# Performance work log

Measured on AMD Instinct MI355X. Metric: run time of the kernel, lower is better.

## Reference

```python
import jax, jax.numpy as jnp
import numpy as np

DEPTH = 9                 # complete binary tree depth
N = 2 ** (DEPTH + 1) - 1  # 1023 nodes per tree (heap layout)
B = 32                    # batch of trees
E = 256                   # word_emb_dims
H = 512                   # treelstm in_dim (cell hidden size)
L = 512                   # decoder LSTM dims
V = 32000                 # vocab size
T = 64                    # max_sequence_length (greedy decode steps)


def setup_inputs() -> dict:
    key = jax.random.key(0)
    ks = jax.random.split(key, 12)
    g = lambda i, shape, s=0.02: jax.random.normal(ks[i], shape, jnp.float32) * s
    return {
        "node_feat": jax.random.randint(ks[0], (B, N), 0, V),
        "mask": jnp.ones((B, N), jnp.int32),
        # shared token embedding (node_emb_layer token_emb, also used by decoder input)
        "emb": g(1, (V, E)),
        # ChildSumTreeLSTMCell params (DGL convention)
        "W_iou": g(2, (E, 3 * H)),
        "U_iou": g(3, (H, 3 * H)),
        "b_iou": jnp.zeros((3 * H,), jnp.float32),
        "U_f_w": g(4, (H, H)),
        "U_f_b": jnp.zeros((H,), jnp.float32),
        # graph-readout -> decoder init state projections
        "hid_fc_w": g(5, (H, L)), "hid_fc_b": jnp.zeros((L,), jnp.float32),
        "cell_fc_w": g(6, (H, L)), "cell_fc_b": jnp.zeros((L,), jnp.float32),
        # decoder LSTMCell (PyTorch gate order i,f,g,o) + vocab projection
        "W_ih": g(7, (E, 4 * L)), "W_hh": g(8, (L, 4 * L)),
        "b_ih": jnp.zeros((4 * L,), jnp.float32), "b_hh": jnp.zeros((4 * L,), jnp.float32),
        "fc_w": g(9, (L, V)), "fc_b": jnp.zeros((V,), jnp.float32),
    }


def _forward(node_feat, mask, emb, W_iou, U_iou, b_iou, U_f_w, U_f_b,
             hid_fc_w, hid_fc_b, cell_fc_w, cell_fc_b,
             W_ih, W_hh, b_ih, b_hh, fc_w, fc_b):
    x = emb[node_feat]                                        # [B,N,E]
    iou_in = (x @ W_iou) * mask[..., None].astype(x.dtype)    # [B,N,3H]
    h = jnp.zeros((B, N, H), x.dtype)
    c = jnp.zeros((B, N, H), x.dtype)

    def apply_node(iou_node, c_agg):
        i, o, u = jnp.split(iou_node + b_iou, 3, axis=-1)
        i, o, u = jax.nn.sigmoid(i), jax.nn.sigmoid(o), jnp.tanh(u)
        c_new = i * u + c_agg
        return o * jnp.tanh(c_new), c_new

    # leaves first (no children -> zero aggregated cell)
    leaf = jnp.arange(2 ** DEPTH - 1, N)
    h_l, c_l = apply_node(iou_in[:, leaf], jnp.zeros((), x.dtype))
    h = h.at[:, leaf].set(h_l)
    c = c.at[:, leaf].set(c_l)

    # level-batched topological propagation (dgl.prop_nodes_topo)
    for d in range(DEPTH - 1, -1, -1):
        idx = jnp.arange(2 ** d - 1, 2 ** (d + 1) - 1)        # nodes at level d
        ch = jnp.stack([2 * idx + 1, 2 * idx + 2], axis=1)    # [n_d,2]
        h_ch, c_ch = h[:, ch], c[:, ch]                       # [B,n_d,2,H]
        h_tild = h_ch.sum(2)                                  # child-sum
        f = jax.nn.sigmoid(h_ch @ U_f_w + U_f_b)              # per-child forget gate
        c_agg = (f * c_ch).sum(2)
        h_n, c_n = apply_node(iou_in[:, idx] + h_tild @ U_iou, c_agg)
        h = h.at[:, idx].set(h_n)
        c = c.at[:, idx].set(c_n)

    mean_feats = h.mean(1)                                    # mean graph readout [B,H]
    hid = mean_feats @ hid_fc_w + hid_fc_b
    cel = mean_feats @ cell_fc_w + cell_fc_b

    def step(carry, _):
        inp, hs, cs = carry
        xt = emb[inp]                                         # [B,E]
        gates = xt @ W_ih + hs @ W_hh + b_ih + b_hh
        ig, fg, gg, og = jnp.split(gates, 4, axis=-1)
        cs = jax.nn.sigmoid(fg) * cs + jax.nn.sigmoid(ig) * jnp.tanh(gg)
        hs = jax.nn.sigmoid(og) * jnp.tanh(cs)
        logits = hs @ fc_w + fc_b                             # [B,V]
        top1 = jnp.argmax(logits, axis=-1)                    # greedy feedback
        return (top1, hs, cs), logits

    inp0 = jnp.zeros((B,), node_feat.dtype)
    _, logits_seq = jax.lax.scan(step, (inp0, hid, cel), None, length=T - 1)
    # t=0 row stays zeros, matching logits_output initialization
    return jnp.concatenate([jnp.zeros((1, B, V), x.dtype), logits_seq], axis=0)


def reference(node_feat, mask, emb, W_iou, U_iou, b_iou, U_f_w, U_f_b,
              hid_fc_w, hid_fc_b, cell_fc_w, cell_fc_b,
              W_ih, W_hh, b_ih, b_hh, fc_w, fc_b):
    return _forward(node_feat, mask, emb, W_iou, U_iou, b_iou, U_f_w, U_f_b,
                    hid_fc_w, hid_fc_b, cell_fc_w, cell_fc_b,
                    W_ih, W_hh, b_ih, b_hh, fc_w, fc_b)
```

## Files before the change

kernel.cpp:

```cpp
#include <hip/hip_runtime.h>
#include <math.h>

#define B_ 32
#define N_ 1023
#define E_ 256
#define H_ 512
#define V_ 32000
#define T_ 64
#define NBL 250

__device__ __forceinline__ float sigf(float x) { return 1.0f / (1.0f + expf(-x)); }

template<bool LEAF>
__global__ void __launch_bounds__(256)
iou_gemm_k(const int* __restrict__ node_feat, const int* __restrict__ mask,
           const float* __restrict__ emb, const float* __restrict__ Wiou,
           const float* __restrict__ Uiou, const float* __restrict__ hbuf,
           float* __restrict__ iou_out, int first, int n, int nshift)
{
    const int rows = B_ * n;
    const int K = LEAF ? E_ : (E_ + H_);
    const int rt = blockIdx.x, ct = blockIdx.y;
    const int tid = threadIdx.x;
    const int tr = tid >> 4, tc = tid & 15;

    __shared__ __align__(16) float As[8][136];
    __shared__ __align__(16) float Bs[8][136];

    float acc[8][8];
#pragma unroll
    for (int i = 0; i < 8; ++i)
#pragma unroll
        for (int j = 0; j < 8; ++j) acc[i][j] = 0.0f;

    const int lrow = tid >> 1;
    const int lkq  = (tid & 1) << 2;
    const int grow = rt * 128 + lrow;
    const bool rvalid = grow < rows;
    int tok = 0; float mval = 0.0f; int hoff1 = 0, hoff2 = 0;
    if (rvalid) {
        const int b = grow >> nshift, j = grow & (n - 1);
        const int node = first + j;
        tok  = node_feat[b * N_ + node];
        mval = (float)mask[b * N_ + node];
        if (!LEAF) {
            hoff1 = (b * N_ + 2 * node + 1) * H_;
            hoff2 = hoff1 + H_;
        }
    }
    const int bk   = tid >> 5;
    const int bcol = (tid & 31) << 2;
    const int gcol = ct * 128 + bcol;

    const int nkt = K >> 3;
    for (int kt = 0; kt < nkt; ++kt) {
        const int k0 = kt << 3;
        {
            const int kg = k0 + lkq;
            float4 v = make_float4(0.f, 0.f, 0.f, 0.f);
            if (rvalid) {
                if (LEAF || kg < E_) {
                    float4 e = *(const float4*)(emb + tok * E_ + kg);
                    v.x = e.x * mval; v.y = e.y * mval; v.z = e.z * mval; v.w = e.w * mval;
                } else {
                    const int kk = kg - E_;
                    float4 h1 = *(const float4*)(hbuf + hoff1 + kk);
                    float4 h2 = *(const float4*)(hbuf + hoff2 + kk);
                    v.x = h1.x + h2.x; v.y = h1.y + h2.y;
                    v.z = h1.z + h2.z; v.w = h1.w + h2.w;
                }
            }
            As[lkq + 0][lrow] = v.x;
            As[lkq + 1][lrow] = v.y;
            As[lkq + 2][lrow] = v.z;
            As[lkq + 3][lrow] = v.w;
        }
        {
            const int kg = k0 + bk;
            const float* src = (LEAF || kg < E_) ? (Wiou + kg * 1536 + gcol)
                                                 : (Uiou + (kg - E_) * 1536 + gcol);
            *(float4*)&Bs[bk][bcol] = *(const float4*)src;
        }
        __syncthreads();
#pragma unroll
        for (int kk = 0; kk < 8; ++kk) {
            float a[8], bb[8];
            *(float4*)&a[0]  = *(const float4*)&As[kk][tr << 3];
            *(float4*)&a[4]  = *(const float4*)&As[kk][(tr << 3) + 4];
            *(float4*)&bb[0] = *(const float4*)&Bs[kk][tc << 2];
            *(float4*)&bb[4] = *(const float4*)&Bs[kk][(tc << 2) + 64];
#pragma unroll
            for (int i = 0; i < 8; ++i)
#pragma unroll
                for (int j = 0; j < 8; ++j)
                    acc[i][j] = fmaf(a[i], bb[j], acc[i][j]);
        }
        __syncthreads();
    }
#pragma unroll
    for (int i = 0; i < 8; ++i) {
        const int r = rt * 128 + (tr << 3) + i;
        if (r < rows) {
            float* dst = iou_out + (size_t)r * 1536 + ct * 128;
            *(float4*)(dst + (tc << 2))      = make_float4(acc[i][0], acc[i][1], acc[i][2], acc[i][3]);
            *(float4*)(dst + 64 + (tc << 2)) = make_float4(acc[i][4], acc[i][5], acc[i][6], acc[i][7]);
        }
    }
}

__global__ void __launch_bounds__(256)
iou_small_k(const int* __restrict__ node_feat, const int* __restrict__ mask,
            const float* __restrict__ emb, const float* __restrict__ Wiou,
            const float* __restrict__ Uiou, const float* __restrict__ hbuf,
            float* __restrict__ iou_out, int first, int n, int nshift)
{
    const int rows = B_ * n;
    const int rt = blockIdx.x, ct = blockIdx.y;
    const int tid = threadIdx.x;
    const int tr = tid >> 4, tc = tid & 15;

    __shared__ __align__(16) float As[8][72];
    __shared__ __align__(16) float Bs[8][72];

    float acc[4][4];
#pragma unroll
    for (int i = 0; i < 4; ++i)
#pragma unroll
        for (int j = 0; j < 4; ++j) acc[i][j] = 0.0f;

    const int srow = tid & 63, skq = tid >> 6;
    const int grow = rt * 64 + srow;
    const bool rvalid = grow < rows;
    int tok = 0; float mval = 0.f; int hoff1 = 0, hoff2 = 0;
    if (rvalid) {
        const int b = grow >> nshift, j = grow & (n - 1);
        const int node = first + j;
        tok  = node_feat[b * N_ + node];
        mval = (float)mask[b * N_ + node];
        hoff1 = (b * N_ + 2 * node + 1) * H_;
        hoff2 = hoff1 + H_;
    }
    const int gcol = ct * 64 + srow;

    for (int kt = 0; kt < 96; ++kt) {
        const int k0 = kt << 3;
        {
            const int kg = k0 + (skq << 1);
            float2 v = make_float2(0.f, 0.f);
            if (rvalid) {
                if (kg < E_) {
                    float2 e = *(const float2*)(emb + tok * E_ + kg);
                    v.x = e.x * mval; v.y = e.y * mval;
                } else {
                    const int kk = kg - E_;
                    float2 h1 = *(const float2*)(hbuf + hoff1 + kk);
                    float2 h2 = *(const float2*)(hbuf + hoff2 + kk);
                    v.x = h1.x + h2.x; v.y = h1.y + h2.y;
                }
            }
            As[(skq << 1) + 0][srow] = v.x;
            As[(skq << 1) + 1][srow] = v.y;
        }
        {
            const int kg = k0 + (skq << 1);
            const float* s0 = (kg < E_) ? (Wiou + (size_t)kg * 1536 + gcol)
                                        : (Uiou + (size_t)(kg - E_) * 1536 + gcol);
            const float* s1 = ((kg + 1) < E_) ? (Wiou + (size_t)(kg + 1) * 1536 + gcol)
                                              : (Uiou + (size_t)(kg + 1 - E_) * 1536 + gcol);
            Bs[(skq << 1) + 0][srow] = *s0;
            Bs[(skq << 1) + 1][srow] = *s1;
        }
        __syncthreads();
#pragma unroll
        for (int kk = 0; kk < 8; ++kk) {
            float a[4], bb[4];
            *(float4*)&a[0]  = *(const float4*)&As[kk][tr << 2];
            *(float4*)&bb[0] = *(const float4*)&Bs[kk][tc << 2];
#pragma unroll
            for (int i = 0; i < 4; ++i)
#pragma unroll
                for (int j = 0; j < 4; ++j)
                    acc[i][j] = fmaf(a[i], bb[j], acc[i][j]);
        }
        __syncthreads();
    }
#pragma unroll
    for (int i = 0; i < 4; ++i) {
        const int r = rt * 64 + (tr << 2) + i;
        if (r < rows)
            *(float4*)(iou_out + (size_t)r * 1536 + ct * 64 + (tc << 2)) =
                make_float4(acc[i][0], acc[i][1], acc[i][2], acc[i][3]);
    }
}

__global__ void __launch_bounds__(256)
fagg_gemm_k(const float* __restrict__ hbuf, const float* __restrict__ cbuf,
            const float* __restrict__ Ufw, const float* __restrict__ Ufb,
            float* __restrict__ cagg, int first, int n, int nshift)
{
    const int rows = 64 * n;
    const int rt = blockIdx.x, ct = blockIdx.y;
    const int tid = threadIdx.x;
    const int tr = tid >> 4, tc = tid & 15;

    __shared__ __align__(16) float As[8][136];
    __shared__ __align__(16) float Bs[8][136];

    float acc[8][8];
#pragma unroll
    for (int i = 0; i < 8; ++i)
#pragma unroll
        for (int j = 0; j < 8; ++j) acc[i][j] = 0.0f;

    const int lrow = tid >> 1;
    const int lkq  = (tid & 1) << 2;
    const int grow = rt * 128 + lrow;
    const bool rvalid = grow < rows;
    int hoff = 0;
    if (rvalid) {
        const int bj = grow >> 1, s = grow & 1;
        const int b = bj >> nshift, j = bj & (n - 1);
        const int node = first + j;
        hoff = (b * N_ + 2 * node + 1 + s) * H_;
    }
    const int bk   = tid >> 5;
    const int bcol = (tid & 31) << 2;
    const int gcol = ct * 128 + bcol;

    for (int kt = 0; kt < 64; ++kt) {
        const int k0 = kt << 3;
        {
            const int kg = k0 + lkq;
            float4 v = make_float4(0.f, 0.f, 0.f, 0.f);
            if (rvalid) v = *(const float4*)(hbuf + hoff + kg);
            As[lkq + 0][lrow] = v.x;
            As[lkq + 1][lrow] = v.y;
            As[lkq + 2][lrow] = v.z;
            As[lkq + 3][lrow] = v.w;
        }
        {
            const int kg = k0 + bk;
            *(float4*)&Bs[bk][bcol] = *(const float4*)(Ufw + kg * H_ + gcol);
        }
        __syncthreads();
#pragma unroll
        for (int kk = 0; kk < 8; ++kk) {
            float a[8], bb[8];
            *(float4*)&a[0]  = *(const float4*)&As[kk][tr << 3];
            *(float4*)&a[4]  = *(const float4*)&As[kk][(tr << 3) + 4];
            *(float4*)&bb[0] = *(const float4*)&Bs[kk][tc << 2];
            *(float4*)&bb[4] = *(const float4*)&Bs[kk][(tc << 2) + 64];
#pragma unroll
            for (int i = 0; i < 8; ++i)
#pragma unroll
                for (int j = 0; j < 8; ++j)
                    acc[i][j] = fmaf(a[i], bb[j], acc[i][j]);
        }
        __syncthreads();
    }
#pragma unroll
    for (int p = 0; p < 4; ++p) {
        const int r0 = rt * 128 + (tr << 3) + 2 * p;
        if (r0 < rows) {
            const int bj = r0 >> 1;
            const int b = bj >> nshift, j = bj & (n - 1);
            const int node = first + j;
            const float* c1 = cbuf + (b * N_ + 2 * node + 1) * H_ + ct * 128;
            const float* c2 = c1 + H_;
            float* dst = cagg + bj * H_ + ct * 128;
#pragma unroll
            for (int g = 0; g < 2; ++g) {
                const int off = (g ? 64 : 0) + (tc << 2);
                const int jb = g * 4;
                float4 cc1 = *(const float4*)(c1 + off);
                float4 cc2 = *(const float4*)(c2 + off);
                float4 bbv = *(const float4*)(Ufb + ct * 128 + off);
                float4 res;
                res.x = sigf(acc[2*p][jb+0] + bbv.x) * cc1.x + sigf(acc[2*p+1][jb+0] + bbv.x) * cc2.x;
                res.y = sigf(acc[2*p][jb+1] + bbv.y) * cc1.y + sigf(acc[2*p+1][jb+1] + bbv.y) * cc2.y;
                res.z = sigf(acc[2*p][jb+2] + bbv.z) * cc1.z + sigf(acc[2*p+1][jb+2] + bbv.z) * cc2.z;
                res.w = sigf(acc[2*p][jb+3] + bbv.w) * cc1.w + sigf(acc[2*p+1][jb+3] + bbv.w) * cc2.w;
                *(float4*)(dst + off) = res;
            }
        }
    }
}

__global__ void __launch_bounds__(256)
fagg_small_k(const float* __restrict__ hbuf, const float* __restrict__ cbuf,
             const float* __restrict__ Ufw, const float* __restrict__ Ufb,
             float* __restrict__ cagg, int first, int n, int nshift)
{
    const int rows = 64 * n;
    const int rt = blockIdx.x, ct = blockIdx.y;
    const int tid = threadIdx.x;
    const int tr = tid >> 4, tc = tid & 15;

    __shared__ __align__(16) float As[8][72];
    __shared__ __align__(16) float Bs[8][72];

    float acc[4][4];
#pragma unroll
    for (int i = 0; i < 4; ++i)
#pragma unroll
        for (int j = 0; j < 4; ++j) acc[i][j] = 0.0f;

    const int srow = tid & 63, skq = tid >> 6;
    const int grow = rt * 64 + srow;
    const bool rvalid = grow < rows;
    int hoff = 0;
    if (rvalid) {
        const int bj = grow >> 1, s = grow & 1;
        const int b = bj >> nshift, j = bj & (n - 1);
        const int node = first + j;
        hoff = (b * N_ + 2 * node + 1 + s) * H_;
    }
    const int gcol = ct * 64 + srow;

    for (int kt = 0; kt < 64; ++kt) {
        const int k0 = kt << 3;
        {
            const int kg = k0 + (skq << 1);
            float2 v = make_float2(0.f, 0.f);
            if (rvalid) v = *(const float2*)(hbuf + hoff + kg);
            As[(skq << 1) + 0][srow] = v.x;
            As[(skq << 1) + 1][srow] = v.y;
        }
        {
            const int kg = k0 + (skq << 1);
            Bs[(skq << 1) + 0][srow] = Ufw[(size_t)kg * H_ + gcol];
            Bs[(skq << 1) + 1][srow] = Ufw[(size_t)(kg + 1) * H_ + gcol];
        }
        __syncthreads();
#pragma unroll
        for (int kk = 0; kk < 8; ++kk) {
            float a[4], bb[4];
            *(float4*)&a[0]  = *(const float4*)&As[kk][tr << 2];
            *(float4*)&bb[0] = *(const float4*)&Bs[kk][tc << 2];
#pragma unroll
            for (int i = 0; i < 4; ++i)
#pragma unroll
                for (int j = 0; j < 4; ++j)
                    acc[i][j] = fmaf(a[i], bb[j], acc[i][j]);
        }
        __syncthreads();
    }
#pragma unroll
    for (int p = 0; p < 2; ++p) {
        const int r0 = rt * 64 + (tr << 2) + 2 * p;
        if (r0 < rows) {
            const int bj = r0 >> 1;
            const int b = bj >> nshift, j = bj & (n - 1);
            const int node = first + j;
            const float* c1 = cbuf + (b * N_ + 2 * node + 1) * H_ + ct * 64;
            const float* c2 = c1 + H_;
            float* dst = cagg + bj * H_ + ct * 64;
            const int off = tc << 2;
            float4 cc1 = *(const float4*)(c1 + off);
            float4 cc2 = *(const float4*)(c2 + off);
            float4 bbv = *(const float4*)(Ufb + ct * 64 + off);
            float4 res;
            res.x = sigf(acc[2*p][0] + bbv.x) * cc1.x + sigf(acc[2*p+1][0] + bbv.x) * cc2.x;
            res.y = sigf(acc[2*p][1] + bbv.y) * cc1.y + sigf(acc[2*p+1][1] + bbv.y) * cc2.y;
            res.z = sigf(acc[2*p][2] + bbv.z) * cc1.z + sigf(acc[2*p+1][2] + bbv.z) * cc2.z;
            res.w = sigf(acc[2*p][3] + bbv.w) * cc1.w + sigf(acc[2*p+1][3] + bbv.w) * cc2.w;
            *(float4*)(dst + off) = res;
        }
    }
}

template<bool LEAF>
__global__ void apply_node_k(const float* __restrict__ iou,
                             const float* __restrict__ b_iou,
                             const float* __restrict__ cagg,
                             float* __restrict__ hbuf, float* __restrict__ cbuf,
                             int first, int n, int nshift)
{
    const int gid = blockIdx.x * 256 + threadIdx.x;
    if (gid >= B_ * n * 128) return;
    const int r = gid >> 7, col = (gid & 127) << 2;
    const float* row = iou + (size_t)r * 1536;
    float4 iv = *(const float4*)(row + col);
    float4 ov = *(const float4*)(row + 512 + col);
    float4 uv = *(const float4*)(row + 1024 + col);
    float4 bi = *(const float4*)(b_iou + col);
    float4 bo = *(const float4*)(b_iou + 512 + col);
    float4 bu = *(const float4*)(b_iou + 1024 + col);
    float4 ca = make_float4(0.f, 0.f, 0.f, 0.f);
    if (!LEAF) ca = *(const float4*)(cagg + r * H_ + col);
    float4 cn, hn;
    cn.x = sigf(iv.x + bi.x) * tanhf(uv.x + bu.x) + ca.x;
    cn.y = sigf(iv.y + bi.y) * tanhf(uv.y + bu.y) + ca.y;
    cn.z = sigf(iv.z + bi.z) * tanhf(uv.z + bu.z) + ca.z;
    cn.w = sigf(iv.w + bi.w) * tanhf(uv.w + bu.w) + ca.w;
    hn.x = sigf(ov.x + bo.x) * tanhf(cn.x);
    hn.y = sigf(ov.y + bo.y) * tanhf(cn.y);
    hn.z = sigf(ov.z + bo.z) * tanhf(cn.z);
    hn.w = sigf(ov.w + bo.w) * tanhf(cn.w);
    const int b = r >> nshift, j = r & (n - 1);
    const int node = first + j;
    const size_t o = (size_t)(b * N_ + node) * H_ + col;
    *(float4*)(cbuf + o) = cn;
    *(float4*)(hbuf + o) = hn;
}

__global__ void mean_part_k(const float* __restrict__ hbuf, float* __restrict__ mpart)
{
    const int bid = blockIdx.x;
    const int b = bid >> 3, chunk = bid & 7;
    const int tid = threadIdx.x;
    const int n0 = chunk * 128;
    const int n1 = (n0 + 128 < N_) ? (n0 + 128) : N_;
    float s0 = 0.f, s1 = 0.f;
    for (int nn = n0; nn < n1; ++nn) {
        const float* p = hbuf + (size_t)(b * N_ + nn) * H_;
        s0 += p[tid];
        s1 += p[tid + 256];
    }
    mpart[(bid << 9) + tid]       = s0;
    mpart[(bid << 9) + tid + 256] = s1;
}

__global__ void mean_fin_k(const float* __restrict__ mpart, float* __restrict__ mf)
{
    const int gid = blockIdx.x * 256 + threadIdx.x;
    const int b = gid >> 9, k = gid & 511;
    float s = 0.f;
#pragma unroll
    for (int c = 0; c < 8; ++c) s += mpart[(((b << 3) + c) << 9) + k];
    mf[gid] = s * (1.0f / 1023.0f);
}

__global__ void hidcel_k(const float* __restrict__ mf,
                         const float* __restrict__ hw, const float* __restrict__ hb,
                         const float* __restrict__ cw, const float* __restrict__ cb,
                         float* __restrict__ hs0, float* __restrict__ cs)
{
    const int gid = blockIdx.x * 256 + threadIdx.x;
    const int which = gid >> 14;
    const int b = (gid >> 9) & 31, l = gid & 511;
    const float* W = which ? cw : hw;
    float acc = which ? cb[l] : hb[l];
#pragma unroll 8
    for (int k = 0; k < H_; ++k) acc = fmaf(mf[b * H_ + k], W[k * H_ + l], acc);
    if (which) cs[b * H_ + l] = acc; else hs0[b * H_ + l] = acc;
}

__global__ void __launch_bounds__(256)
wtrans_k(const float* __restrict__ W_ih, const float* __restrict__ W_hh,
         float* __restrict__ Wt)
{
    __shared__ float t[64][33];
    const int k0 = blockIdx.x * 32;
    const int g0 = blockIdx.y * 64;
    const int tid = threadIdx.x;
    for (int idx = tid; idx < 2048; idx += 256) {
        const int kk = idx >> 6, gg = idx & 63;
        const int k = k0 + kk;
        t[gg][kk] = (k < E_) ? W_ih[(size_t)k * 2048 + g0 + gg]
                             : W_hh[(size_t)(k - E_) * 2048 + g0 + gg];
    }
    __syncthreads();
    for (int idx = tid; idx < 2048; idx += 256) {
        const int gg = idx >> 5, kk = idx & 31;
        Wt[(size_t)(g0 + gg) * 768 + k0 + kk] = t[gg][kk];
    }
}

__global__ void __launch_bounds__(256)
lstm_step_k(const float* __restrict__ emb, const float* __restrict__ Wt,
            const float* __restrict__ b_ih, const float* __restrict__ b_hh,
            const float* __restrict__ pval, const int* __restrict__ pidx,
            const float* __restrict__ hs_in, float* __restrict__ hs_out,
            float* __restrict__ cs, int t)
{
    __shared__ __align__(16) float xh[8][776];
    __shared__ __align__(16) float part[4][8][8][4];
    __shared__ float rv[256];
    __shared__ int   ri[256];
    __shared__ int   tokS[8];
    const int tid = threadIdx.x;
    const int bg  = blockIdx.y;

    if (t == 1) {
        if (tid < 8) tokS[tid] = 0;
    } else {
        const int bs = tid >> 5, th = tid & 31;
        const int b = bg * 8 + bs;
        float bv = -INFINITY; int bi = 0x7fffffff;
        for (int p = th; p < NBL; p += 32) {
            const float v = pval[b * NBL + p];
            const int  ix = pidx[b * NBL + p];
            if (v > bv || (v == bv && ix < bi)) { bv = v; bi = ix; }
        }
        rv[tid] = bv; ri[tid] = bi;
        __syncthreads();
        if (tid < 8) {
            float Bv = -INFINITY; int Bi = 0x7fffffff;
#pragma unroll
            for (int c = 0; c < 32; ++c) {
                const float v = rv[tid * 32 + c];
                const int  ix = ri[tid * 32 + c];
                if (v > Bv || (v == Bv && ix < Bi)) { Bv = v; Bi = ix; }
            }
            tokS[tid] = Bi;
        }
    }
    __syncthreads();

    for (int idx = tid; idx < 8 * E_; idx += 256) {
        const int b = idx >> 8, k = idx & 255;
        xh[b][k] = emb[(size_t)tokS[b] * E_ + k];
    }
    for (int idx = tid; idx < 8 * H_; idx += 256) {
        const int b = idx >> 9, k = idx & 511;
        xh[b][E_ + k] = hs_in[(size_t)(bg * 8 + b) * H_ + k];
    }
    __syncthreads();

    const int ks = tid >> 6;
    const int lane = tid & 63;
    const int bi = lane >> 3, li = lane & 7;
    const int l = blockIdx.x * 8 + li;
    float ai = 0.f, af = 0.f, ag = 0.f, ao = 0.f;
    const int k0 = ks * 192;
    const float* wi = Wt + (size_t)(l)        * 768 + k0;
    const float* wf = Wt + (size_t)(512 + l)  * 768 + k0;
    const float* wg = Wt + (size_t)(1024 + l) * 768 + k0;
    const float* wo = Wt + (size_t)(1536 + l) * 768 + k0;
    const float* xp = &xh[bi][k0];
#pragma unroll 4
    for (int kk = 0; kk < 192; kk += 4) {
        const float4 xv = *(const float4*)(xp + kk);
        const float4 w0 = *(const float4*)(wi + kk);
        const float4 w1 = *(const float4*)(wf + kk);
        const float4 w2 = *(const float4*)(wg + kk);
        const float4 w3 = *(const float4*)(wo + kk);
        ai = fmaf(xv.x, w0.x, ai); ai = fmaf(xv.y, w0.y, ai);
        ai = fmaf(xv.z, w0.z, ai); ai = fmaf(xv.w, w0.w, ai);
        af = fmaf(xv.x, w1.x, af); af = fmaf(xv.y, w1.y, af);
        af = fmaf(xv.z, w1.z, af); af = fmaf(xv.w, w1.w, af);
        ag = fmaf(xv.x, w2.x, ag); ag = fmaf(xv.y, w2.y, ag);
        ag = fmaf(xv.z, w2.z, ag); ag = fmaf(xv.w, w2.w, ag);
        ao = fmaf(xv.x, w3.x, ao); ao = fmaf(xv.y, w3.y, ao);
        ao = fmaf(xv.z, w3.z, ao); ao = fmaf(xv.w, w3.w, ao);
    }
    part[ks][bi][li][0] = ai;
    part[ks][bi][li][1] = af;
    part[ks][bi][li][2] = ag;
    part[ks][bi][li][3] = ao;
    __syncthreads();

    if (tid < 64) {
        const int b2 = tid >> 3, l2i = tid & 7;
        const int l2 = blockIdx.x * 8 + l2i;
        const int b = bg * 8 + b2;
        float s0 = 0.f, s1 = 0.f, s2 = 0.f, s3 = 0.f;
#pragma unroll
        for (int q = 0; q < 4; ++q) {
            s0 += part[q][b2][l2i][0];
            s1 += part[q][b2][l2i][1];
            s2 += part[q][b2][l2i][2];
            s3 += part[q][b2][l2i][3];
        }
        const float gi = s0 + b_ih[l2]        + b_hh[l2];
        const float gf = s1 + b_ih[512 + l2]  + b_hh[512 + l2];
        const float gg = s2 + b_ih[1024 + l2] + b_hh[1024 + l2];
        const float go = s3 + b_ih[1536 + l2] + b_hh[1536 + l2];
        const float co = cs[b * H_ + l2];
        const float cn = sigf(gf) * co + sigf(gi) * tanhf(gg);
        cs[b * H_ + l2] = cn;
        hs_out[b * H_ + l2] = sigf(go) * tanhf(cn);
    }
}

__global__ void __launch_bounds__(256)
logits_part_k(const float* __restrict__ fc_w, const float* __restrict__ hs,
              float* __restrict__ partial)
{
    __shared__ __align__(16) float sm[256 * 36];
    const int tid = threadIdx.x;
    const int blk = blockIdx.x;
    const int kh  = blockIdx.y;

    for (int idx = tid; idx < B_ * 256; idx += 256) {
        const int b = idx & 31, k = idx >> 5;
        sm[k * 36 + b] = hs[b * H_ + kh * 256 + k];
    }
    __syncthreads();

    const int w8   = (tid >> 6) << 3;
    const int lane = tid & 63;
    const int col  = (blk << 7) + (lane << 1);

    float acc[8][2];
#pragma unroll
    for (int i = 0; i < 8; ++i) { acc[i][0] = 0.f; acc[i][1] = 0.f; }

    const float* wp = fc_w + (size_t)(kh * 256) * V_ + col;
    const float* hp = sm + w8;
    float2 wreg[8];
#pragma unroll
    for (int j = 0; j < 8; ++j) wreg[j] = *(const float2*)(wp + (size_t)j * V_);
    for (int kb = 0; kb < 32; ++kb) {
        float2 wnxt[8];
        if (kb < 31) {
            const float* wq = wp + (size_t)((kb + 1) << 3) * V_;
#pragma unroll
            for (int j = 0; j < 8; ++j) wnxt[j] = *(const float2*)(wq + (size_t)j * V_);
        }
#pragma unroll
        for (int j = 0; j < 8; ++j) {
            const float* hq = hp + ((kb << 3) + j) * 36;
            float hv[8];
            *(float4*)&hv[0] = *(const float4*)(hq);
            *(float4*)&hv[4] = *(const float4*)(hq + 4);
#pragma unroll
            for (int i = 0; i < 8; ++i) {
                acc[i][0] = fmaf(hv[i], wreg[j].x, acc[i][0]);
                acc[i][1] = fmaf(hv[i], wreg[j].y, acc[i][1]);
            }
        }
        if (kb < 31) {
#pragma unroll
            for (int j = 0; j < 8; ++j) wreg[j] = wnxt[j];
        }
    }
#pragma unroll
    for (int i = 0; i < 8; ++i) {
        float* dst = partial + (size_t)(kh * B_ + w8 + i) * V_ + col;
        *(float2*)dst = make_float2(acc[i][0], acc[i][1]);
    }
}

__global__ void __launch_bounds__(256)
logits_fin_k(const float* __restrict__ partial, const float* __restrict__ fc_b,
             float* __restrict__ out_t, float* __restrict__ pval,
             int* __restrict__ pidx)
{
    __shared__ float rv[256];
    __shared__ int   ri[256];
    const int tid = threadIdx.x, blk = blockIdx.x;
    const int b = tid >> 3, cg = (tid & 7) << 4;
    const int colbase = (blk << 7) + cg;

    const float* p0 = partial + (size_t)b * V_ + colbase;
    const float* p1 = partial + (size_t)(B_ + b) * V_ + colbase;
    const float* bp = fc_b + colbase;
    float* op = out_t + (size_t)b * V_ + colbase;

    float bv = -INFINITY; int bi = 0;
#pragma unroll
    for (int q = 0; q < 4; ++q) {
        float4 a = *(const float4*)(p0 + (q << 2));
        float4 c = *(const float4*)(p1 + (q << 2));
        float4 d = *(const float4*)(bp + (q << 2));
        float4 v;
        v.x = a.x + c.x + d.x; v.y = a.y + c.y + d.y;
        v.z = a.z + c.z + d.z; v.w = a.w + c.w + d.w;
        *(float4*)(op + (q << 2)) = v;
        const int c0 = cg + (q << 2);
        if (v.x > bv) { bv = v.x; bi = c0 + 0; }
        if (v.y > bv) { bv = v.y; bi = c0 + 1; }
        if (v.z > bv) { bv = v.z; bi = c0 + 2; }
        if (v.w > bv) { bv = v.w; bi = c0 + 3; }
    }
    rv[tid] = bv; ri[tid] = bi;
    __syncthreads();
    if (tid < B_) {
        float Bv = -INFINITY; int Bi = 0;
#pragma unroll
        for (int q = 0; q < 8; ++q) {
            const float v = rv[(tid << 3) + q];
            if (v > Bv) { Bv = v; Bi = ri[(tid << 3) + q]; }
        }
        pval[tid * NBL + blk] = Bv;
        pidx[tid * NBL + blk] = (blk << 7) + Bi;
    }
}

extern "C" void kernel_launch(void* const* d_in, const int* in_sizes, int n_in,
                              void* d_out, int out_size, void* d_ws, size_t ws_size,
                              hipStream_t stream)
{
    (void)in_sizes; (void)n_in; (void)out_size; (void)ws_size;
    const int*   node_feat = (const int*)  d_in[0];
    const int*   mask      = (const int*)  d_in[1];
    const float* emb       = (const float*)d_in[2];
    const float* W_iou     = (const float*)d_in[3];
    const float* U_iou     = (const float*)d_in[4];
    const float* b_iou     = (const float*)d_in[5];
    const float* U_f_w     = (const float*)d_in[6];
    const float* U_f_b     = (const float*)d_in[7];
    const float* hid_fc_w  = (const float*)d_in[8];
    const float* hid_fc_b  = (const float*)d_in[9];
    const float* cell_fc_w = (const float*)d_in[10];
    const float* cell_fc_b = (const float*)d_in[11];
    const float* W_ih      = (const float*)d_in[12];
    const float* W_hh      = (const float*)d_in[13];
    const float* b_ih      = (const float*)d_in[14];
    const float* b_hh      = (const float*)d_in[15];
    const float* fc_w      = (const float*)d_in[16];
    const float* fc_b      = (const float*)d_in[17];
    float* out = (float*)d_out;

    float* ws      = (float*)d_ws;
    float* iou_buf = ws;
    float* cagg    = ws + 12582912;
    float* hbuf    = ws + 16777216;
    float* cbuf    = ws + 33538048;
    float* mf      = ws + 50298880;
    float* hsb     = ws + 50315264;
    float* csb     = ws + 50348032;
    float* pval    = ws + 50364416;
    int*   pidx    = (int*)(ws + 50372416);
    float* mpart   = iou_buf;
    float* partial = iou_buf + 262144;
    float* Wt      = iou_buf + 2359296;

    for (int chunk = 0; chunk < 2; ++chunk) {
        const int first = 511 + 256 * chunk;
        dim3 g(64, 12);
        iou_gemm_k<true><<<g, 256, 0, stream>>>(node_feat, mask, emb, W_iou, U_iou,
                                                hbuf, iou_buf, first, 256, 8);
        apply_node_k<true><<<4096, 256, 0, stream>>>(iou_buf, b_iou, cagg,
                                                     hbuf, cbuf, first, 256, 8);
    }
    for (int d = 8; d >= 0; --d) {
        const int n = 1 << d, first = n - 1;
        if (n <= 64) {
            dim3 gf((64 * n + 63) / 64, 8);
            fagg_small_k<<<gf, 256, 0, stream>>>(hbuf, cbuf, U_f_w, U_f_b, cagg, first, n, d);
            dim3 gi((32 * n + 63) / 64, 24);
            iou_small_k<<<gi, 256, 0, stream>>>(node_feat, mask, emb, W_iou, U_iou,
                                                hbuf, iou_buf, first, n, d);
        } else {
            dim3 gf((64 * n + 127) / 128, 4);
            fagg_gemm_k<<<gf, 256, 0, stream>>>(hbuf, cbuf, U_f_w, U_f_b, cagg, first, n, d);
            dim3 gi((32 * n + 127) / 128, 12);
            iou_gemm_k<false><<<gi, 256, 0, stream>>>(node_feat, mask, emb, W_iou, U_iou,
                                                      hbuf, iou_buf, first, n, d);
        }
        apply_node_k<false><<<16 * n, 256, 0, stream>>>(iou_buf, b_iou, cagg,
                                                        hbuf, cbuf, first, n, d);
    }
    mean_part_k<<<256, 256, 0, stream>>>(hbuf, mpart);
    mean_fin_k<<<64, 256, 0, stream>>>(mpart, mf);
    hidcel_k<<<128, 256, 0, stream>>>(mf, hid_fc_w, hid_fc_b, cell_fc_w, cell_fc_b, hsb, csb);
    dim3 gw(24, 32);
    wtrans_k<<<gw, 256, 0, stream>>>(W_ih, W_hh, Wt);
    hipMemsetAsync(d_out, 0, (size_t)B_ * V_ * sizeof(float), stream);
    for (int t = 1; t < T_; ++t) {
        const float* hs_in  = hsb + ((t - 1) & 1) * (B_ * H_);
        float*       hs_out = hsb + (t & 1) * (B_ * H_);
        dim3 gl(64, 4);
        lstm_step_k<<<gl, 256, 0, stream>>>(emb, Wt, b_ih, b_hh,
                                            pval, pidx, hs_in, hs_out, csb, t);
        dim3 gp(NBL, 2);
        logits_part_k<<<gp, 256, 0, stream>>>(fc_w, hs_out, partial);
        logits_fin_k<<<NBL, 256, 0, stream>>>(partial, fc_b,
                                              out + (size_t)t * B_ * V_, pval, pidx);
    }
}
```

Before: 5.996 ms.

## Fuse iou GEMM with node apply and use nontemporal logits stores

```diff
diff --git a/kernel.cpp b/kernel.cpp
--- a/kernel.cpp
+++ b/kernel.cpp
@@ -11,12 +11,21 @@
 
 __device__ __forceinline__ float sigf(float x) { return 1.0f / (1.0f + expf(-x)); }
 
+__device__ __forceinline__ void nt_store4(float* p, float4 v)
+{
+    __builtin_nontemporal_store(v.x, p + 0);
+    __builtin_nontemporal_store(v.y, p + 1);
+    __builtin_nontemporal_store(v.z, p + 2);
+    __builtin_nontemporal_store(v.w, p + 3);
+}
+
 template<bool LEAF>
 __global__ void __launch_bounds__(256)
-iou_gemm_k(const int* __restrict__ node_feat, const int* __restrict__ mask,
-           const float* __restrict__ emb, const float* __restrict__ Wiou,
-           const float* __restrict__ Uiou, const float* __restrict__ hbuf,
-           float* __restrict__ iou_out, int first, int n, int nshift)
+iou_apply_k(const int* __restrict__ node_feat, const int* __restrict__ mask,
+            const float* __restrict__ emb, const float* __restrict__ Wiou,
+            const float* __restrict__ Uiou, const float* __restrict__ b_iou,
+            const float* __restrict__ cagg, float* __restrict__ hbuf,
+            float* __restrict__ cbuf, int first, int n, int nshift)
 {
     const int rows = B_ * n;
     const int K = LEAF ? E_ : (E_ + H_);
@@ -24,20 +33,19 @@
     const int tid = threadIdx.x;
     const int tr = tid >> 4, tc = tid & 15;
 
-    __shared__ __align__(16) float As[8][136];
-    __shared__ __align__(16) float Bs[8][136];
-
-    float acc[8][8];
-#pragma unroll
-    for (int i = 0; i < 8; ++i)
-#pragma unroll
-        for (int j = 0; j < 8; ++j) acc[i][j] = 0.0f;
-
-    const int lrow = tid >> 1;
-    const int lkq  = (tid & 1) << 2;
-    const int grow = rt * 128 + lrow;
+    __shared__ __align__(16) float As[8][72];
+    __shared__ __align__(16) float Bs[3][8][136];
+
+    float aI[4][8], aO[4][8], aU[4][8];
+#pragma unroll
+    for (int i = 0; i < 4; ++i)
+#pragma unroll
+        for (int j = 0; j < 8; ++j) { aI[i][j] = 0.f; aO[i][j] = 0.f; aU[i][j] = 0.f; }
+
+    const int srow = tid & 63, skq = tid >> 6;
+    const int grow = rt * 64 + srow;
     const bool rvalid = grow < rows;
-    int tok = 0; float mval = 0.0f; int hoff1 = 0, hoff2 = 0;
+    int tok = 0; float mval = 0.f; int hoff1 = 0, hoff2 = 0;
     if (rvalid) {
         const int b = grow >> nshift, j = grow & (n - 1);
         const int node = first + j;
@@ -56,54 +64,88 @@
     for (int kt = 0; kt < nkt; ++kt) {
         const int k0 = kt << 3;
         {
-            const int kg = k0 + lkq;
-            float4 v = make_float4(0.f, 0.f, 0.f, 0.f);
+            const int kg = k0 + (skq << 1);
+            float2 v = make_float2(0.f, 0.f);
             if (rvalid) {
                 if (LEAF || kg < E_) {
-                    float4 e = *(const float4*)(emb + tok * E_ + kg);
-                    v.x = e.x * mval; v.y = e.y * mval; v.z = e.z * mval; v.w = e.w * mval;
+                    float2 e = *(const float2*)(emb + (size_t)tok * E_ + kg);
+                    v.x = e.x * mval; v.y = e.y * mval;
                 } else {
                     const int kk = kg - E_;
-                    float4 h1 = *(const float4*)(hbuf + hoff1 + kk);
-                    float4 h2 = *(const float4*)(hbuf + hoff2 + kk);
+                    float2 h1 = *(const float2*)(hbuf + hoff1 + kk);
+                    float2 h2 = *(const float2*)(hbuf + hoff2 + kk);
                     v.x = h1.x + h2.x; v.y = h1.y + h2.y;
-                    v.z = h1.z + h2.z; v.w = h1.w + h2.w;
                 }
             }
-            As[lkq + 0][lrow] = v.x;
-            As[lkq + 1][lrow] = v.y;
-            As[lkq + 2][lrow] = v.z;
-            As[lkq + 3][lrow] = v.w;
+            As[(skq << 1) + 0][srow] = v.x;
+            As[(skq << 1) + 1][srow] = v.y;
         }
         {
             const int kg = k0 + bk;
-            const float* src = (LEAF || kg < E_) ? (Wiou + kg * 1536 + gcol)
-                                                 : (Uiou + (kg - E_) * 1536 + gcol);
-            *(float4*)&Bs[bk][bcol] = *(const float4*)src;
+            const float* src = (LEAF || kg < E_) ? (Wiou + (size_t)kg * 1536)
+                                                 : (Uiou + (size_t)(kg - E_) * 1536);
+            *(float4*)&Bs[0][bk][bcol] = *(const float4*)(src + gcol);
+            *(float4*)&Bs[1][bk][bcol] = *(const float4*)(src + 512 + gcol);
+            *(float4*)&Bs[2][bk][bcol] = *(const float4*)(src + 1024 + gcol);
         }
         __syncthreads();
 #pragma unroll
         for (int kk = 0; kk < 8; ++kk) {
-            float a[8], bb[8];
-            *(float4*)&a[0]  = *(const float4*)&As[kk][tr << 3];
-            *(float4*)&a[4]  = *(const float4*)&As[kk][(tr << 3) + 4];
-            *(float4*)&bb[0] = *(const float4*)&Bs[kk][tc << 2];
-            *(float4*)&bb[4] = *(const float4*)&Bs[kk][(tc << 2) + 64];
-#pragma unroll
-            for (int i = 0; i < 8; ++i)
-#pragma unroll
-                for (int j = 0; j < 8; ++j)
-                    acc[i][j] = fmaf(a[i], bb[j], acc[i][j]);
+            float a[4];
+            *(float4*)&a[0] = *(const float4*)&As[kk][tr << 2];
+            float bI[8], bO[8], bU[8];
+            *(float4*)&bI[0] = *(const float4*)&Bs[0][kk][tc << 3];
+            *(float4*)&bI[4] = *(const float4*)&Bs[0][kk][(tc << 3) + 4];
+            *(float4*)&bO[0] = *(const float4*)&Bs[1][kk][tc << 3];
+            *(float4*)&bO[4] = *(const float4*)&Bs[1][kk][(tc << 3) + 4];
+            *(float4*)&bU[0] = *(const float4*)&Bs[2][kk][tc << 3];
+            *(float4*)&bU[4] = *(const float4*)&Bs[2][kk][(tc << 3) + 4];
+#pragma unroll
+            for (int i = 0; i < 4; ++i)
+#pragma unroll
+                for (int j = 0; j < 8; ++j) {
+                    aI[i][j] = fmaf(a[i], bI[j], aI[i][j]);
+                    aO[i][j] = fmaf(a[i], bO[j], aO[i][j]);
+                    aU[i][j] = fmaf(a[i], bU[j], aU[i][j]);
+                }
         }
         __syncthreads();
     }
-#pragma unroll
-    for (int i = 0; i < 8; ++i) {
-        const int r = rt * 128 + (tr << 3) + i;
+
+    const int cbase = ct * 128 + (tc << 3);
+    float bI[8], bO[8], bU[8];
+    *(float4*)&bI[0] = *(const float4*)(b_iou + cbase);
+    *(float4*)&bI[4] = *(const float4*)(b_iou + cbase + 4);
+    *(float4*)&bO[0] = *(const float4*)(b_iou + 512 + cbase);
+    *(float4*)&bO[4] = *(const float4*)(b_iou + 512 + cbase + 4);
+    *(float4*)&bU[0] = *(const float4*)(b_iou + 1024 + cbase);
+    *(float4*)&bU[4] = *(const float4*)(b_iou + 1024 + cbase + 4);
+
+#pragma unroll
+    for (int p = 0; p < 4; ++p) {
+        const int r = rt * 64 + (tr << 2) + p;
         if (r < rows) {
-            float* dst = iou_out + (size_t)r * 1536 + ct * 128;
-            *(float4*)(dst + (tc << 2))      = make_float4(acc[i][0], acc[i][1], acc[i][2], acc[i][3]);
-            *(float4*)(dst + 64 + (tc << 2)) = make_float4(acc[i][4], acc[i][5], acc[i][6], acc[i][7]);
+            const int b = r >> nshift, j = r & (n - 1);
+            const int node = first + j;
+            float ca[8];
+            if (LEAF) {
+#pragma unroll
+                for (int e = 0; e < 8; ++e) ca[e] = 0.f;
+            } else {
+                *(float4*)&ca[0] = *(const float4*)(cagg + (size_t)r * H_ + cbase);
+                *(float4*)&ca[4] = *(const float4*)(cagg + (size_t)r * H_ + cbase + 4);
+            }
+            float cn[8], hn[8];
+#pragma unroll
+            for (int e = 0; e < 8; ++e) {
+                cn[e] = sigf(aI[p][e] + bI[e]) * tanhf(aU[p][e] + bU[e]) + ca[e];
+                hn[e] = sigf(aO[p][e] + bO[e]) * tanhf(cn[e]);
+            }
+            const size_t o = (size_t)(b * N_ + node) * H_ + cbase;
+            *(float4*)(cbuf + o)     = *(float4*)&cn[0];
+            *(float4*)(cbuf + o + 4) = *(float4*)&cn[4];
+            *(float4*)(hbuf + o)     = *(float4*)&hn[0];
+            *(float4*)(hbuf + o + 4) = *(float4*)&hn[4];
         }
     }
 }
@@ -369,7 +411,6 @@
     }
 }
 
-template<bool LEAF>
 __global__ void apply_node_k(const float* __restrict__ iou,
                              const float* __restrict__ b_iou,
                              const float* __restrict__ cagg,
@@ -386,8 +427,7 @@
     float4 bi = *(const float4*)(b_iou + col);
     float4 bo = *(const float4*)(b_iou + 512 + col);
     float4 bu = *(const float4*)(b_iou + 1024 + col);
-    float4 ca = make_float4(0.f, 0.f, 0.f, 0.f);
-    if (!LEAF) ca = *(const float4*)(cagg + r * H_ + col);
+    float4 ca = *(const float4*)(cagg + r * H_ + col);
     float4 cn, hn;
     cn.x = sigf(iv.x + bi.x) * tanhf(uv.x + bu.x) + ca.x;
     cn.y = sigf(iv.y + bi.y) * tanhf(uv.y + bu.y) + ca.y;
@@ -658,7 +698,7 @@
         float4 v;
         v.x = a.x + c.x + d.x; v.y = a.y + c.y + d.y;
         v.z = a.z + c.z + d.z; v.w = a.w + c.w + d.w;
-        *(float4*)(op + (q << 2)) = v;
+        nt_store4(op + (q << 2), v);
         const int c0 = cg + (q << 2);
         if (v.x > bv) { bv = v.x; bi = c0 + 0; }
         if (v.y > bv) { bv = v.y; bi = c0 + 1; }
@@ -714,17 +754,14 @@
     float* csb     = ws + 50348032;
     float* pval    = ws + 50364416;
     int*   pidx    = (int*)(ws + 50372416);
-    float* mpart   = iou_buf;
-    float* partial = iou_buf + 262144;
-    float* Wt      = iou_buf + 2359296;
-
-    for (int chunk = 0; chunk < 2; ++chunk) {
-        const int first = 511 + 256 * chunk;
-        dim3 g(64, 12);
-        iou_gemm_k<true><<<g, 256, 0, stream>>>(node_feat, mask, emb, W_iou, U_iou,
-                                                hbuf, iou_buf, first, 256, 8);
-        apply_node_k<true><<<4096, 256, 0, stream>>>(iou_buf, b_iou, cagg,
-                                                     hbuf, cbuf, first, 256, 8);
+    float* mpart   = iou_buf + 4194304;
+    float* partial = iou_buf + 4325376;
+    float* Wt      = iou_buf + 6373376;
+
+    {
+        dim3 g(256, 4);
+        iou_apply_k<true><<<g, 256, 0, stream>>>(node_feat, mask, emb, W_iou, U_iou,
+                                                 b_iou, cagg, hbuf, cbuf, 511, 512, 9);
     }
     for (int d = 8; d >= 0; --d) {
         const int n = 1 << d, first = n - 1;
@@ -734,15 +771,15 @@
             dim3 gi((32 * n + 63) / 64, 24);
             iou_small_k<<<gi, 256, 0, stream>>>(node_feat, mask, emb, W_iou, U_iou,
                                                 hbuf, iou_buf, first, n, d);
+            apply_node_k<<<16 * n, 256, 0, stream>>>(iou_buf, b_iou, cagg,
+                                                     hbuf, cbuf, first, n, d);
         } else {
             dim3 gf((64 * n + 127) / 128, 4);
             fagg_gemm_k<<<gf, 256, 0, stream>>>(hbuf, cbuf, U_f_w, U_f_b, cagg, first, n, d);
-            dim3 gi((32 * n + 127) / 128, 12);
-            iou_gemm_k<false><<<gi, 256, 0, stream>>>(node_feat, mask, emb, W_iou, U_iou,
-                                                      hbuf, iou_buf, first, n, d);
-        }
-        apply_node_k<false><<<16 * n, 256, 0, stream>>>(iou_buf, b_iou, cagg,
-                                                        hbuf, cbuf, first, n, d);
+            dim3 gi((32 * n + 63) / 64, 4);
+            iou_apply_k<false><<<gi, 256, 0, stream>>>(node_feat, mask, emb, W_iou, U_iou,
+                                                       b_iou, cagg, hbuf, cbuf, first, n, d);
+        }
     }
     mean_part_k<<<256, 256, 0, stream>>>(hbuf, mpart);
     mean_fin_k<<<64, 256, 0, stream>>>(mpart, mf);
```

After: 6.035 ms. No clear change (+0.7%).

## Merge forget-gate and iou GEMMs per tree level into one launch

Applied to the files above, without the earlier changes.

```diff
diff --git a/kernel.cpp b/kernel.cpp
--- a/kernel.cpp
+++ b/kernel.cpp
@@ -11,21 +11,27 @@
 
 __device__ __forceinline__ float sigf(float x) { return 1.0f / (1.0f + expf(-x)); }
 
+__device__ __forceinline__ void nt_store4(float* p, float4 v)
+{
+    __builtin_nontemporal_store(v.x, p + 0);
+    __builtin_nontemporal_store(v.y, p + 1);
+    __builtin_nontemporal_store(v.z, p + 2);
+    __builtin_nontemporal_store(v.w, p + 3);
+}
+
+
 template<bool LEAF>
-__global__ void __launch_bounds__(256)
-iou_gemm_k(const int* __restrict__ node_feat, const int* __restrict__ mask,
-           const float* __restrict__ emb, const float* __restrict__ Wiou,
-           const float* __restrict__ Uiou, const float* __restrict__ hbuf,
-           float* __restrict__ iou_out, int first, int n, int nshift)
+__device__ __forceinline__ void iou_body(
+    const int* __restrict__ node_feat, const int* __restrict__ mask,
+    const float* __restrict__ emb, const float* __restrict__ Wiou,
+    const float* __restrict__ Uiou, const float* __restrict__ hbuf,
+    float* __restrict__ iou_out, int first, int n, int nshift,
+    int rt, int ct, float (*As)[136], float (*Bs)[136])
 {
     const int rows = B_ * n;
     const int K = LEAF ? E_ : (E_ + H_);
-    const int rt = blockIdx.x, ct = blockIdx.y;
     const int tid = threadIdx.x;
     const int tr = tid >> 4, tc = tid & 15;
-
-    __shared__ __align__(16) float As[8][136];
-    __shared__ __align__(16) float Bs[8][136];
 
     float acc[8][8];
 #pragma unroll
@@ -108,19 +114,106 @@
     }
 }
 
-__global__ void __launch_bounds__(256)
-iou_small_k(const int* __restrict__ node_feat, const int* __restrict__ mask,
-            const float* __restrict__ emb, const float* __restrict__ Wiou,
-            const float* __restrict__ Uiou, const float* __restrict__ hbuf,
-            float* __restrict__ iou_out, int first, int n, int nshift)
-{
-    const int rows = B_ * n;
-    const int rt = blockIdx.x, ct = blockIdx.y;
+__device__ __forceinline__ void fagg_body(
+    const float* __restrict__ hbuf, const float* __restrict__ cbuf,
+    const float* __restrict__ Ufw, const float* __restrict__ Ufb,
+    float* __restrict__ cagg, int first, int n, int nshift,
+    int rt, int ct, float (*As)[136], float (*Bs)[136])
+{
+    const int rows = 64 * n;
     const int tid = threadIdx.x;
     const int tr = tid >> 4, tc = tid & 15;
 
-    __shared__ __align__(16) float As[8][72];
-    __shared__ __align__(16) float Bs[8][72];
+    float acc[8][8];
+#pragma unroll
+    for (int i = 0; i < 8; ++i)
+#pragma unroll
+        for (int j = 0; j < 8; ++j) acc[i][j] = 0.0f;
+
+    const int lrow = tid >> 1;
+    const int lkq  = (tid & 1) << 2;
+    const int grow = rt * 128 + lrow;
+    const bool rvalid = grow < rows;
+    int hoff = 0;
+    if (rvalid) {
+        const int bj = grow >> 1, s = grow & 1;
+        const int b = bj >> nshift, j = bj & (n - 1);
+        const int node = first + j;
+        hoff = (b * N_ + 2 * node + 1 + s) * H_;
+    }
+    const int bk   = tid >> 5;
+    const int bcol = (tid & 31) << 2;
+    const int gcol = ct * 128 + bcol;
+
+    for (int kt = 0; kt < 64; ++kt) {
+        const int k0 = kt << 3;
+        {
+            const int kg = k0 + lkq;
+            float4 v = make_float4(0.f, 0.f, 0.f, 0.f);
+            if (rvalid) v = *(const float4*)(hbuf + hoff + kg);
+            As[lkq + 0][lrow] = v.x;
+            As[lkq + 1][lrow] = v.y;
+            As[lkq + 2][lrow] = v.z;
+            As[lkq + 3][lrow] = v.w;
+        }
+        {
+            const int kg = k0 + bk;
+            *(float4*)&Bs[bk][bcol] = *(const float4*)(Ufw + kg * H_ + gcol);
+        }
+        __syncthreads();
+#pragma unroll
+        for (int kk = 0; kk < 8; ++kk) {
+            float a[8], bb[8];
+            *(float4*)&a[0]  = *(const float4*)&As[kk][tr << 3];
+            *(float4*)&a[4]  = *(const float4*)&As[kk][(tr << 3) + 4];
+            *(float4*)&bb[0] = *(const float4*)&Bs[kk][tc << 2];
+            *(float4*)&bb[4] = *(const float4*)&Bs[kk][(tc << 2) + 64];
+#pragma unroll
+            for (int i = 0; i < 8; ++i)
+#pragma unroll
+                for (int j = 0; j < 8; ++j)
+                    acc[i][j] = fmaf(a[i], bb[j], acc[i][j]);
+        }
+        __syncthreads();
+    }
+#pragma unroll
+    for (int p = 0; p < 4; ++p) {
+        const int r0 = rt * 128 + (tr << 3) + 2 * p;
+        if (r0 < rows) {
+            const int bj = r0 >> 1;
+            const int b = bj >> nshift, j = bj & (n - 1);
+            const int node = first + j;
+            const float* c1 = cbuf + (b * N_ + 2 * node + 1) * H_ + ct * 128;
+            const float* c2 = c1 + H_;
+            float* dst = cagg + bj * H_ + ct * 128;
+#pragma unroll
+            for (int g = 0; g < 2; ++g) {
+                const int off = (g ? 64 : 0) + (tc << 2);
+                const int jb = g * 4;
+                float4 cc1 = *(const float4*)(c1 + off);
+                float4 cc2 = *(const float4*)(c2 + off);
+                float4 bbv = *(const float4*)(Ufb + ct * 128 + off);
+                float4 res;
+                res.x = sigf(acc[2*p][jb+0] + bbv.x) * cc1.x + sigf(acc[2*p+1][jb+0] + bbv.x) * cc2.x;
+                res.y = sigf(acc[2*p][jb+1] + bbv.y) * cc1.y + sigf(acc[2*p+1][jb+1] + bbv.y) * cc2.y;
+                res.z = sigf(acc[2*p][jb+2] + bbv.z) * cc1.z + sigf(acc[2*p+1][jb+2] + bbv.z) * cc2.z;
+                res.w = sigf(acc[2*p][jb+3] + bbv.w) * cc1.w + sigf(acc[2*p+1][jb+3] + bbv.w) * cc2.w;
+                *(float4*)(dst + off) = res;
+            }
+        }
+    }
+}
+
+__device__ __forceinline__ void iou_small_body(
+    const int* __restrict__ node_feat, const int* __restrict__ mask,
+    const float* __restrict__ emb, const float* __restrict__ Wiou,
+    const float* __restrict__ Uiou, const float* __restrict__ hbuf,
+    float* __restrict__ iou_out, int first, int n, int nshift,
+    int rt, int ct, float (*As)[72], float (*Bs)[72])
+{
+    const int rows = B_ * n;
+    const int tid = threadIdx.x;
+    const int tr = tid >> 4, tc = tid & 15;
 
     float acc[4][4];
 #pragma unroll
@@ -193,111 +286,15 @@
     }
 }
 
-__global__ void __launch_bounds__(256)
-fagg_gemm_k(const float* __restrict__ hbuf, const float* __restrict__ cbuf,
-            const float* __restrict__ Ufw, const float* __restrict__ Ufb,
-            float* __restrict__ cagg, int first, int n, int nshift)
+__device__ __forceinline__ void fagg_small_body(
+    const float* __restrict__ hbuf, const float* __restrict__ cbuf,
+    const float* __restrict__ Ufw, const float* __restrict__ Ufb,
+    float* __restrict__ cagg, int first, int n, int nshift,
+    int rt, int ct, float (*As)[72], float (*Bs)[72])
 {
     const int rows = 64 * n;
-    const int rt = blockIdx.x, ct = blockIdx.y;
     const int tid = threadIdx.x;
     const int tr = tid >> 4, tc = tid & 15;
-
-    __shared__ __align__(16) float As[8][136];
-    __shared__ __align__(16) float Bs[8][136];
-
-    float acc[8][8];
-#pragma unroll
-    for (int i = 0; i < 8; ++i)
-#pragma unroll
-        for (int j = 0; j < 8; ++j) acc[i][j] = 0.0f;
-
-    const int lrow = tid >> 1;
-    const int lkq  = (tid & 1) << 2;
-    const int grow = rt * 128 + lrow;
-    const bool rvalid = grow < rows;
-    int hoff = 0;
-    if (rvalid) {
-        const int bj = grow >> 1, s = grow & 1;
-        const int b = bj >> nshift, j = bj & (n - 1);
-        const int node = first + j;
-        hoff = (b * N_ + 2 * node + 1 + s) * H_;
-    }
-    const int bk   = tid >> 5;
-    const int bcol = (tid & 31) << 2;
-    const int gcol = ct * 128 + bcol;
-
-    for (int kt = 0; kt < 64; ++kt) {
-        const int k0 = kt << 3;
-        {
-            const int kg = k0 + lkq;
-            float4 v = make_float4(0.f, 0.f, 0.f, 0.f);
-            if (rvalid) v = *(const float4*)(hbuf + hoff + kg);
-            As[lkq + 0][lrow] = v.x;
-            As[lkq + 1][lrow] = v.y;
-            As[lkq + 2][lrow] = v.z;
-            As[lkq + 3][lrow] = v.w;
-        }
-        {
-            const int kg = k0 + bk;
-            *(float4*)&Bs[bk][bcol] = *(const float4*)(Ufw + kg * H_ + gcol);
-        }
-        __syncthreads();
-#pragma unroll
-        for (int kk = 0; kk < 8; ++kk) {
-            float a[8], bb[8];
-            *(float4*)&a[0]  = *(const float4*)&As[kk][tr << 3];
-            *(float4*)&a[4]  = *(const float4*)&As[kk][(tr << 3) + 4];
-            *(float4*)&bb[0] = *(const float4*)&Bs[kk][tc << 2];
-            *(float4*)&bb[4] = *(const float4*)&Bs[kk][(tc << 2) + 64];
-#pragma unroll
-            for (int i = 0; i < 8; ++i)
-#pragma unroll
-                for (int j = 0; j < 8; ++j)
-                    acc[i][j] = fmaf(a[i], bb[j], acc[i][j]);
-        }
-        __syncthreads();
-    }
-#pragma unroll
-    for (int p = 0; p < 4; ++p) {
-        const int r0 = rt * 128 + (tr << 3) + 2 * p;
-        if (r0 < rows) {
-            const int bj = r0 >> 1;
-            const int b = bj >> nshift, j = bj & (n - 1);
-            const int node = first + j;
-            const float* c1 = cbuf + (b * N_ + 2 * node + 1) * H_ + ct * 128;
-            const float* c2 = c1 + H_;
-            float* dst = cagg + bj * H_ + ct * 128;
-#pragma unroll
-            for (int g = 0; g < 2; ++g) {
-                const int off = (g ? 64 : 0) + (tc << 2);
-                const int jb = g * 4;
-                float4 cc1 = *(const float4*)(c1 + off);
-                float4 cc2 = *(const float4*)(c2 + off);
-                float4 bbv = *(const float4*)(Ufb + ct * 128 + off);
-                float4 res;
-                res.x = sigf(acc[2*p][jb+0] + bbv.x) * cc1.x + sigf(acc[2*p+1][jb+0] + bbv.x) * cc2.x;
-                res.y = sigf(acc[2*p][jb+1] + bbv.y) * cc1.y + sigf(acc[2*p+1][jb+1] + bbv.y) * cc2.y;
-                res.z = sigf(acc[2*p][jb+2] + bbv.z) * cc1.z + sigf(acc[2*p+1][jb+2] + bbv.z) * cc2.z;
-                res.w = sigf(acc[2*p][jb+3] + bbv.w) * cc1.w + sigf(acc[2*p+1][jb+3] + bbv.w) * cc2.w;
-                *(float4*)(dst + off) = res;
-            }
-        }
-    }
-}
-
-__global__ void __launch_bounds__(256)
-fagg_small_k(const float* __restrict__ hbuf, const float* __restrict__ cbuf,
-             const float* __restrict__ Ufw, const float* __restrict__ Ufb,
-             float* __restrict__ cagg, int first, int n, int nshift)
-{
-    const int rows = 64 * n;
-    const int rt = blockIdx.x, ct = blockIdx.y;
-    const int tid = threadIdx.x;
-    const int tr = tid >> 4, tc = tid & 15;
-
-    __shared__ __align__(16) float As[8][72];
-    __shared__ __align__(16) float Bs[8][72];
 
     float acc[4][4];
 #pragma unroll
@@ -366,6 +363,68 @@
             res.w = sigf(acc[2*p][3] + bbv.w) * cc1.w + sigf(acc[2*p+1][3] + bbv.w) * cc2.w;
             *(float4*)(dst + off) = res;
         }
+    }
+}
+
+
+template<bool LEAF>
+__global__ void __launch_bounds__(256)
+iou_gemm_k(const int* __restrict__ node_feat, const int* __restrict__ mask,
+           const float* __restrict__ emb, const float* __restrict__ Wiou,
+           const float* __restrict__ Uiou, const float* __restrict__ hbuf,
+           float* __restrict__ iou_out, int first, int n, int nshift)
+{
+    __shared__ __align__(16) float As[8][136];
+    __shared__ __align__(16) float Bs[8][136];
+    iou_body<LEAF>(node_feat, mask, emb, Wiou, Uiou, hbuf, iou_out,
+                   first, n, nshift, blockIdx.x, blockIdx.y, As, Bs);
+}
+
+__global__ void __launch_bounds__(256)
+tree_big_k(const int* __restrict__ node_feat, const int* __restrict__ mask,
+           const float* __restrict__ emb, const float* __restrict__ Wiou,
+           const float* __restrict__ Uiou, const float* __restrict__ hbuf,
+           const float* __restrict__ cbuf, const float* __restrict__ Ufw,
+           const float* __restrict__ Ufb, float* __restrict__ cagg,
+           float* __restrict__ iou_out, int first, int n, int nshift)
+{
+    __shared__ __align__(16) float As[8][136];
+    __shared__ __align__(16) float Bs[8][136];
+    const int nf_rt = n >> 1;
+    const int Nf    = nf_rt << 2;
+    const int bid   = blockIdx.x;
+    if (bid < Nf) {
+        fagg_body(hbuf, cbuf, Ufw, Ufb, cagg, first, n, nshift,
+                  bid % nf_rt, bid / nf_rt, As, Bs);
+    } else {
+        const int b2 = bid - Nf;
+        const int ni_rt = n >> 2;
+        iou_body<false>(node_feat, mask, emb, Wiou, Uiou, hbuf, iou_out,
+                        first, n, nshift, b2 % ni_rt, b2 / ni_rt, As, Bs);
+    }
+}
+
+__global__ void __launch_bounds__(256)
+tree_small_k(const int* __restrict__ node_feat, const int* __restrict__ mask,
+             const float* __restrict__ emb, const float* __restrict__ Wiou,
+             const float* __restrict__ Uiou, const float* __restrict__ hbuf,
+             const float* __restrict__ cbuf, const float* __restrict__ Ufw,
+             const float* __restrict__ Ufb, float* __restrict__ cagg,
+             float* __restrict__ iou_out, int first, int n, int nshift)
+{
+    __shared__ __align__(16) float As[8][72];
+    __shared__ __align__(16) float Bs[8][72];
+    const int nf_rt = n;
+    const int Nf    = nf_rt << 3;
+    const int bid   = blockIdx.x;
+    if (bid < Nf) {
+        fagg_small_body(hbuf, cbuf, Ufw, Ufb, cagg, first, n, nshift,
+                        bid % nf_rt, bid / nf_rt, As, Bs);
+    } else {
+        const int b2 = bid - Nf;
+        const int ni_rt = (n >= 2) ? (n >> 1) : 1;
+        iou_small_body(node_feat, mask, emb, Wiou, Uiou, hbuf, iou_out,
+                       first, n, nshift, b2 % ni_rt, b2 / ni_rt, As, Bs);
     }
 }
 
@@ -658,7 +717,7 @@
         float4 v;
         v.x = a.x + c.x + d.x; v.y = a.y + c.y + d.y;
         v.z = a.z + c.z + d.z; v.w = a.w + c.w + d.w;
-        *(float4*)(op + (q << 2)) = v;
+        nt_store4(op + (q << 2), v);
         const int c0 = cg + (q << 2);
         if (v.x > bv) { bv = v.x; bi = c0 + 0; }
         if (v.y > bv) { bv = v.y; bi = c0 + 1; }
@@ -728,18 +787,17 @@
     }
     for (int d = 8; d >= 0; --d) {
         const int n = 1 << d, first = n - 1;
-        if (n <= 64) {
-            dim3 gf((64 * n + 63) / 64, 8);
-            fagg_small_k<<<gf, 256, 0, stream>>>(hbuf, cbuf, U_f_w, U_f_b, cagg, first, n, d);
-            dim3 gi((32 * n + 63) / 64, 24);
-            iou_small_k<<<gi, 256, 0, stream>>>(node_feat, mask, emb, W_iou, U_iou,
-                                                hbuf, iou_buf, first, n, d);
+        if (n >= 128) {
+            const int nb = (n >> 1) * 4 + (n >> 2) * 12;
+            tree_big_k<<<nb, 256, 0, stream>>>(node_feat, mask, emb, W_iou, U_iou,
+                                               hbuf, cbuf, U_f_w, U_f_b, cagg,
+                                               iou_buf, first, n, d);
         } else {
-            dim3 gf((64 * n + 127) / 128, 4);
-            fagg_gemm_k<<<gf, 256, 0, stream>>>(hbuf, cbuf, U_f_w, U_f_b, cagg, first, n, d);
-            dim3 gi((32 * n + 127) / 128, 12);
-            iou_gemm_k<false><<<gi, 256, 0, stream>>>(node_feat, mask, emb, W_iou, U_iou,
-                                                      hbuf, iou_buf, first, n, d);
+            const int ni_rt = (n >= 2) ? (n >> 1) : 1;
+            const int nb = n * 8 + ni_rt * 24;
+            tree_small_k<<<nb, 256, 0, stream>>>(node_feat, mask, emb, W_iou, U_iou,
+                                                 hbuf, cbuf, U_f_w, U_f_b, cagg,
+                                                 iou_buf, first, n, d);
         }
         apply_node_k<false><<<16 * n, 256, 0, stream>>>(iou_buf, b_iou, cagg,
                                                         hbuf, cbuf, first, n, d);
```

Measured after the change: 5.911 ms. Within noise of the previous version (-1.4%).
